# Kernel optimization log

Hardware: AMD Instinct MI355X
Metric: run time of the kernel (lower is better)

## Reference

```python
import jax, jax.numpy as jnp
import numpy as np
import math

B, T, D, H = 2, 2048, 1024, 16


def _layernorm(x, gamma, beta, eps=1e-5):
    mu = jnp.mean(x, axis=-1, keepdims=True)
    var = jnp.var(x, axis=-1, keepdims=True)
    return (x - mu) * jax.lax.rsqrt(var + eps) * gamma + beta


def setup_inputs() -> dict:
    key = jax.random.key(0)
    ks = jax.random.split(key, 12)
    s = 1.0 / math.sqrt(D)
    return {
        "x": jax.random.normal(ks[0], (B, T, D), dtype=jnp.float32),
        "src_mask": jax.random.randint(ks[1], (B, T, T), 0, 2, dtype=jnp.int32),
        "ln_gamma": jnp.ones((D,), jnp.float32),
        "ln_beta": jnp.zeros((D,), jnp.float32),
        "Wq": jax.random.normal(ks[2], (D, D), jnp.float32) * s,
        "bq": jnp.zeros((D,), jnp.float32),
        "Wk": jax.random.normal(ks[3], (D, D), jnp.float32) * s,
        "bk": jnp.zeros((D,), jnp.float32),
        "Wv": jax.random.normal(ks[4], (D, D), jnp.float32) * s,
        "bv": jnp.zeros((D,), jnp.float32),
        "Wo": jax.random.normal(ks[5], (D, D), jnp.float32) * s,
        "bo": jnp.zeros((D,), jnp.float32),
    }


def reference(x, src_mask, ln_gamma, ln_beta, Wq, bq, Wk, bk, Wv, bv, Wo, bo):
    Bx, Tx, Dx = x.shape
    dh = Dx // H
    xn = _layernorm(x, ln_gamma, ln_beta)  # single LN; the three calls are identical
    q = (xn @ Wq + bq).reshape(Bx, Tx, H, dh)
    k = (xn @ Wk + bk).reshape(Bx, Tx, H, dh)
    v = (xn @ Wv + bv).reshape(Bx, Tx, H, dh)
    # scores: B, n, m, h
    attn = jnp.einsum('bnhd,bmhd->bnmh', q, k) / math.sqrt(dh)
    attn = attn + (1.0 - src_mask.astype(attn.dtype))[..., None] * -100000.0
    weight = jax.nn.softmax(attn, axis=2)
    y = jnp.einsum('bnmh,bmhd->bnhd', weight, v).reshape(Bx, Tx, Dx)
    return x + (y @ Wo + bo)
```

## Files before the change

kernel.cpp:

```cpp
#include <hip/hip_runtime.h>
#include <hip/hip_bf16.h>
#include <stdint.h>

#define Tq 2048
#define Dd 1024
#define Hh 16

typedef unsigned short u16;
typedef __attribute__((ext_vector_type(8))) short short8;
typedef __attribute__((ext_vector_type(4))) float f32x4;

__device__ __forceinline__ u16 f2bf(float f) {
  union { float f; unsigned u; } v; v.f = f;
  unsigned r = (v.u + 0x7fffu + ((v.u >> 16) & 1u)) >> 16;
  return (u16)r;
}

__device__ __forceinline__ unsigned pk2bf(float a, float b) {
  __hip_bfloat162 h = __float22bfloat162_rn(float2{a, b});
  union { __hip_bfloat162 h; unsigned u; } c; c.h = h;
  return c.u;
}

__device__ __forceinline__ void load_lds16(const void* g, void* l) {
  __builtin_amdgcn_global_load_lds(
      (const __attribute__((address_space(1))) unsigned*)g,
      (__attribute__((address_space(3))) unsigned*)l, 16, 0, 0);
}

__device__ __forceinline__ f32x4 mfma16(short8 a, short8 b, f32x4 c) {
  return __builtin_amdgcn_mfma_f32_16x16x32_bf16(a, b, c, 0, 0, 0);
}

__global__ __launch_bounds__(256) void prep_kernel(
    const float* __restrict__ x, const float* __restrict__ gamma,
    const float* __restrict__ beta, u16* __restrict__ xn,
    const float* __restrict__ W0, const float* __restrict__ W1,
    const float* __restrict__ W2, const float* __restrict__ W3,
    u16* __restrict__ o_qkv, u16* __restrict__ o_o,
    const int* __restrict__ mask, uint32_t* __restrict__ bits,
    const float* __restrict__ bq, const float* __restrict__ bk,
    const float* __restrict__ bv, float* __restrict__ bias3) {
  __shared__ float t[32][33];
  int idx = blockIdx.x;
  int tid = threadIdx.x;
  if (idx < 4096) {
    int row = idx;
    const float4 v = ((const float4*)(x + (size_t)row * Dd))[tid];
    float s = v.x + v.y + v.z + v.w;
    float s2 = v.x * v.x + v.y * v.y + v.z * v.z + v.w * v.w;
#pragma unroll
    for (int off = 1; off < 64; off <<= 1) {
      s += __shfl_xor(s, off);
      s2 += __shfl_xor(s2, off);
    }
    int w = tid >> 6;
    if ((tid & 63) == 0) { t[0][w] = s; t[0][4 + w] = s2; }
    __syncthreads();
    s = t[0][0] + t[0][1] + t[0][2] + t[0][3];
    s2 = t[0][4] + t[0][5] + t[0][6] + t[0][7];
    float mu = s * (1.0f / Dd);
    float var = s2 * (1.0f / Dd) - mu * mu;
    float rstd = rsqrtf(var + 1e-5f);
    const float4 g = ((const float4*)gamma)[tid];
    const float4 bb = ((const float4*)beta)[tid];
    union { unsigned us[2]; uint2 u2; } o;
    o.us[0] = pk2bf((v.x - mu) * rstd * g.x + bb.x, (v.y - mu) * rstd * g.y + bb.y);
    o.us[1] = pk2bf((v.z - mu) * rstd * g.z + bb.z, (v.w - mu) * rstd * g.w + bb.w);
    *(uint2*)(xn + (size_t)row * Dd + tid * 4) = o.u2;
  } else if (idx < 8192) {
    int ti = idx - 4096;
    int z = ti >> 10, i = ti & 1023;
    const float* W = (z == 0) ? W0 : (z == 1) ? W1 : (z == 2) ? W2 : W3;
    u16* out = (z < 3) ? (o_qkv + (size_t)z * 1024 * 1024) : o_o;
    int k0 = (i & 31) * 32, n0 = (i >> 5) * 32;
    int tx = tid & 31, ty = tid >> 5;
#pragma unroll
    for (int j = 0; j < 4; ++j)
      t[ty + j * 8][tx] = W[(size_t)(k0 + ty + j * 8) * Dd + n0 + tx];
    __syncthreads();
#pragma unroll
    for (int j = 0; j < 4; ++j)
      out[(size_t)(n0 + ty + j * 8) * Dd + k0 + tx] = f2bf(t[tx][ty + j * 8]);
  } else if (idx < 9216) {
    int m = idx - 8192;
    int b = m >> 9, rest = m & 511;
    int qw = rest >> 3, kblk = rest & 7;
    int k = kblk * 256 + tid;
    const int* mp = mask + ((size_t)b * Tq + qw * 32) * Tq + k;
    uint32_t wv = 0;
#pragma unroll
    for (int j = 0; j < 32; ++j) wv |= (mp[(size_t)j * Tq] ? 1u : 0u) << j;
    bits[((size_t)b * 64 + qw) * Tq + k] = wv;
  } else {
    int i = (idx - 9216) * 256 + tid;
    float v = (i < 1024) ? bq[i] : (i < 2048) ? bk[i - 1024] : bv[i - 2048];
    bias3[i] = v;
  }
}

__global__ __launch_bounds__(256) void vt_kernel(
    const u16* __restrict__ qkv, u16* __restrict__ vt) {
  __shared__ u16 t[32][33];
  int bh = blockIdx.z;
  int b = bh >> 4, h = bh & 15;
  int t0 = blockIdx.x * 32, d0 = blockIdx.y * 32;
  int tx = threadIdx.x & 31, ty = threadIdx.x >> 5;
#pragma unroll
  for (int i = 0; i < 4; ++i)
    t[ty + i * 8][tx] =
        qkv[(size_t)(b * Tq + t0 + ty + i * 8) * 3072 + 2048 + h * 64 + d0 + tx];
  __syncthreads();
#pragma unroll
  for (int i = 0; i < 4; ++i)
    vt[((size_t)bh * 64 + d0 + ty + i * 8) * Tq + t0 + tx] = t[tx][ty + i * 8];
}

template <int MODE, int MT>
__global__ __launch_bounds__(256) void gemm_bt(
    const u16* __restrict__ A, const u16* __restrict__ Bt,
    const float* __restrict__ bias, const float* __restrict__ resid,
    void* __restrict__ Cout, int ldc, int K) {
  constexpr int MTI = MT / 32;
  constexpr int ACALLS = MT / 64;
  __shared__ u16 As[MT * 32];
  __shared__ u16 Bs[128 * 32];
  int tid = threadIdx.x;
  int lane = tid & 63, w = tid >> 6;
  int l16 = lane & 15, quad = lane >> 4;
  int wm = w >> 1, wn = w & 1;
  int m0 = blockIdx.y * MT, n0 = blockIdx.x * 128;
  int srow = lane >> 2, scol = (lane & 3) << 3;
  const u16* ga0 = A + (size_t)(m0 + srow) * K + scol;
  const u16* gb0 = Bt + (size_t)(n0 + srow) * K + scol;
  f32x4 acc[MTI][4];
#pragma unroll
  for (int i = 0; i < MTI; ++i)
#pragma unroll
    for (int j = 0; j < 4; ++j) acc[i][j] = {0.f, 0.f, 0.f, 0.f};

  for (int k0 = 0; k0 < K; k0 += 32) {
    __syncthreads();
#pragma unroll
    for (int c = 0; c < ACALLS; ++c) {
      int rb = w * (MT / 4) + c * 16;
      load_lds16(ga0 + (size_t)rb * K + k0, (char*)As + rb * 64);
    }
#pragma unroll
    for (int c = 0; c < 2; ++c) {
      int rb = w * 32 + c * 16;
      load_lds16(gb0 + (size_t)rb * K + k0, (char*)Bs + rb * 64);
    }
    __syncthreads();
    short8 af[MTI], bf[4];
#pragma unroll
    for (int mt = 0; mt < MTI; ++mt)
      af[mt] = *(const short8*)&As[(wm * (MT / 2) + mt * 16 + l16) * 32 + quad * 8];
#pragma unroll
    for (int nt = 0; nt < 4; ++nt)
      bf[nt] = *(const short8*)&Bs[(wn * 64 + nt * 16 + l16) * 32 + quad * 8];
#pragma unroll
    for (int mt = 0; mt < MTI; ++mt)
#pragma unroll
      for (int nt = 0; nt < 4; ++nt)
        acc[mt][nt] = mfma16(af[mt], bf[nt], acc[mt][nt]);
  }
#pragma unroll
  for (int nt = 0; nt < 4; ++nt) {
    int col = n0 + wn * 64 + nt * 16 + l16;
    float bv = bias[col];
    float scl = (MODE == 0 && col < 1024) ? 0.125f : 1.0f;
#pragma unroll
    for (int mt = 0; mt < MTI; ++mt) {
#pragma unroll
      for (int r = 0; r < 4; ++r) {
        int row = m0 + wm * (MT / 2) + mt * 16 + quad * 4 + r;
        size_t idx = (size_t)row * ldc + col;
        float vv = (acc[mt][nt][r] + bv) * scl;
        if (MODE == 0)
          ((u16*)Cout)[idx] = f2bf(vv);
        else
          ((float*)Cout)[idx] = vv + resid[idx];
      }
    }
  }
}

__global__ __launch_bounds__(256, 2) void attn_kernel(
    const u16* __restrict__ qkv, const u16* __restrict__ vt,
    const uint32_t* __restrict__ mbits, u16* __restrict__ ybuf) {
  __shared__ u16 Ks[2][64 * 64];
  __shared__ u16 Vs[2][64 * 64];
  __shared__ u16 Plds[4][32 * 64];
  int tid = threadIdx.x;
  int lane = tid & 63, w = tid >> 6;
  int l16 = lane & 15, quad = lane >> 4;
  int x7 = l16 & 7;
  int qt = blockIdx.x, h = blockIdx.y, b = blockIdx.z;
  int qbase = qt * 128 + w * 32;
  const u16* Qb = qkv + (size_t)b * Tq * 3072 + h * 64;
  const u16* Kb = Qb + 1024;
  const u16* Vb = vt + ((size_t)(b * Hh + h)) * 64 * Tq;
  const uint32_t* Mrow = mbits + ((size_t)b * 64 + (qbase >> 5)) * Tq;
  u16* Pw = Plds[w];

  int half = (w & 1) * 32;
  int r8 = lane >> 3;
  int phys = lane & 7;
  int chunk = phys ^ r8;
  bool isK = (w < 2);

  short8 qf[2][2];
#pragma unroll
  for (int nt = 0; nt < 2; ++nt)
#pragma unroll
    for (int ks = 0; ks < 2; ++ks)
      qf[nt][ks] = *(const short8*)&Qb[(size_t)(qbase + nt * 16 + l16) * 3072 +
                                       ks * 32 + quad * 8];

  f32x4 acc[2][4];
#pragma unroll
  for (int i = 0; i < 2; ++i)
#pragma unroll
    for (int j = 0; j < 4; ++j) acc[i][j] = {0.f, 0.f, 0.f, 0.f};
  float lst[2] = {0.f, 0.f};

  auto stage = [&](int buf, int k0) {
    if (isK) {
#pragma unroll
      for (int j = 0; j < 4; ++j)
        load_lds16(Kb + (size_t)(k0 + half + j * 8 + r8) * 3072 + chunk * 8,
                   (char*)&Ks[buf][0] + (half + j * 8) * 128);
    } else {
#pragma unroll
      for (int j = 0; j < 4; ++j)
        load_lds16(Vb + (size_t)(half + j * 8 + r8) * Tq + k0 + chunk * 8,
                   (char*)&Vs[buf][0] + (half + j * 8) * 128);
    }
  };

  stage(0, 0);

  for (int kt = 0; kt < 32; ++kt) {
    int k0 = kt * 64;
    int buf = kt & 1;
    __syncthreads();
    uint32_t mv[4][4];
#pragma unroll
    for (int mt = 0; mt < 4; ++mt) {
      uint4 m4 = *(const uint4*)&Mrow[k0 + mt * 16 + quad * 4];
      mv[mt][0] = m4.x; mv[mt][1] = m4.y; mv[mt][2] = m4.z; mv[mt][3] = m4.w;
    }
    if (kt < 31) stage(buf ^ 1, k0 + 64);
    const u16* Kt = Ks[buf];
    const u16* Vtile = Vs[buf];
    f32x4 s[4][2];
#pragma unroll
    for (int i = 0; i < 4; ++i)
#pragma unroll
      for (int j = 0; j < 2; ++j) s[i][j] = {0.f, 0.f, 0.f, 0.f};
#pragma unroll
    for (int mt = 0; mt < 4; ++mt)
#pragma unroll
      for (int ks = 0; ks < 2; ++ks) {
        short8 kf = *(const short8*)&Kt[(mt * 16 + l16) * 64 +
                                        (((ks << 2) | quad) ^ x7) * 8];
#pragma unroll
        for (int nt = 0; nt < 2; ++nt)
          s[mt][nt] = mfma16(kf, qf[nt][ks], s[mt][nt]);
      }
#pragma unroll
    for (int nt = 0; nt < 2; ++nt) {
      int shift = nt * 16 + l16;
#pragma unroll
      for (int mt = 0; mt < 4; ++mt) {
#pragma unroll
        for (int r = 0; r < 4; ++r) {
          float sv = ((mv[mt][r] >> shift) & 1u) ? s[mt][nt][r] : -100000.0f;
          float p = __expf(sv);
          s[mt][nt][r] = p;
          lst[nt] += p;
        }
        union { unsigned us[2]; uint2 u2; } pk;
        pk.us[0] = pk2bf(s[mt][nt][0], s[mt][nt][1]);
        pk.us[1] = pk2bf(s[mt][nt][2], s[mt][nt][3]);
        int p16 = (mt * 2 + (quad >> 1)) ^ x7;
        *(uint2*)&Pw[(nt * 16 + l16) * 64 + p16 * 8 + (quad & 1) * 4] = pk.u2;
      }
    }
    short8 pf[2][2];
#pragma unroll
    for (int mt2 = 0; mt2 < 2; ++mt2)
#pragma unroll
      for (int ks = 0; ks < 2; ++ks)
        pf[mt2][ks] = *(const short8*)&Pw[(mt2 * 16 + l16) * 64 +
                                          (((ks << 2) | quad) ^ x7) * 8];
#pragma unroll
    for (int ks = 0; ks < 2; ++ks)
#pragma unroll
      for (int nt2 = 0; nt2 < 4; ++nt2) {
        short8 vf = *(const short8*)&Vtile[(nt2 * 16 + l16) * 64 +
                                           (((ks << 2) | quad) ^ x7) * 8];
#pragma unroll
        for (int mt2 = 0; mt2 < 2; ++mt2)
          acc[mt2][nt2] = mfma16(pf[mt2][ks], vf, acc[mt2][nt2]);
      }
  }
#pragma unroll
  for (int nt = 0; nt < 2; ++nt) {
    lst[nt] += __shfl_xor(lst[nt], 16);
    lst[nt] += __shfl_xor(lst[nt], 32);
  }
#pragma unroll
  for (int mt2 = 0; mt2 < 2; ++mt2)
#pragma unroll
    for (int r = 0; r < 4; ++r) {
      float li = 1.0f / __shfl(lst[mt2], quad * 4 + r);
      size_t row = (size_t)b * Tq + qbase + mt2 * 16 + quad * 4 + r;
#pragma unroll
      for (int nt2 = 0; nt2 < 4; ++nt2)
        ybuf[row * Dd + h * 64 + nt2 * 16 + l16] = f2bf(acc[mt2][nt2][r] * li);
    }
}

extern "C" void kernel_launch(void* const* d_in, const int* in_sizes, int n_in,
                              void* d_out, int out_size, void* d_ws, size_t ws_size,
                              hipStream_t stream) {
  (void)in_sizes; (void)n_in; (void)out_size; (void)ws_size;
  const float* x = (const float*)d_in[0];
  const int* mask = (const int*)d_in[1];
  const float* gamma = (const float*)d_in[2];
  const float* beta = (const float*)d_in[3];
  const float* Wq = (const float*)d_in[4];
  const float* bq = (const float*)d_in[5];
  const float* Wk = (const float*)d_in[6];
  const float* bk = (const float*)d_in[7];
  const float* Wv = (const float*)d_in[8];
  const float* bv = (const float*)d_in[9];
  const float* Wo = (const float*)d_in[10];
  const float* bo = (const float*)d_in[11];
  float* out = (float*)d_out;
  char* ws = (char*)d_ws;

  constexpr size_t SZ_XN = (size_t)4096 * 1024 * 2;
  constexpr size_t SZ_WTQ = (size_t)3072 * 1024 * 2;
  constexpr size_t SZ_WOT = (size_t)1024 * 1024 * 2;
  constexpr size_t SZ_B3 = 3072 * 4;
  constexpr size_t SZ_QKV = (size_t)4096 * 3072 * 2;
  constexpr size_t SZ_MBITS = (size_t)2 * 64 * 2048 * 4;
  constexpr size_t SZ_VT = (size_t)2 * 16 * 64 * 2048 * 2;
  size_t off = 0;
  u16* xn = (u16*)(ws + off); off += SZ_XN;
  u16* wtqkv = (u16*)(ws + off); off += SZ_WTQ;
  u16* wot = (u16*)(ws + off); off += SZ_WOT;
  float* bias3 = (float*)(ws + off); off += SZ_B3;
  u16* qkvb = (u16*)(ws + off); off += SZ_QKV;
  uint32_t* mbits = (uint32_t*)(ws + off); off += SZ_MBITS;
  u16* vtb = (u16*)(ws + off); off += SZ_VT;
  u16* ybuf = (u16*)(ws + off);

  prep_kernel<<<dim3(9228), dim3(256), 0, stream>>>(
      x, gamma, beta, xn, Wq, Wk, Wv, Wo, wtqkv, wot, mask, mbits, bq, bk, bv,
      bias3);
  gemm_bt<0, 128><<<dim3(24, 32), dim3(256), 0, stream>>>(
      xn, wtqkv, bias3, nullptr, qkvb, 3072, 1024);
  vt_kernel<<<dim3(64, 2, 32), dim3(256), 0, stream>>>(qkvb, vtb);
  attn_kernel<<<dim3(16, 16, 2), dim3(256), 0, stream>>>(qkvb, vtb, mbits, ybuf);
  gemm_bt<1, 64><<<dim3(8, 64), dim3(256), 0, stream>>>(
      ybuf, wot, bo, x, out, 1024, 1024);
}
```

Baseline: 246.0 us.

## Split attention over key halves, add combine kernel, widen GEMM K-tile

Measured after the change: 255.9 us. +4.0%, slower.

```diff
diff --git a/kernel.cpp b/kernel.cpp
--- a/kernel.cpp
+++ b/kernel.cpp
@@ -122,54 +122,66 @@
     const float* __restrict__ bias, const float* __restrict__ resid,
     void* __restrict__ Cout, int ldc, int K) {
   constexpr int MTI = MT / 32;
-  constexpr int ACALLS = MT / 64;
-  __shared__ u16 As[MT * 32];
-  __shared__ u16 Bs[128 * 32];
+  __shared__ u16 As[MT * 64];
+  __shared__ u16 Bs[128 * 64];
   int tid = threadIdx.x;
   int lane = tid & 63, w = tid >> 6;
   int l16 = lane & 15, quad = lane >> 4;
+  int x7 = l16 & 7;
   int wm = w >> 1, wn = w & 1;
   int m0 = blockIdx.y * MT, n0 = blockIdx.x * 128;
-  int srow = lane >> 2, scol = (lane & 3) << 3;
-  const u16* ga0 = A + (size_t)(m0 + srow) * K + scol;
-  const u16* gb0 = Bt + (size_t)(n0 + srow) * K + scol;
+  int r8 = lane >> 3;
+  int phys = lane & 7;
+  int chunk = phys ^ r8;
+  const u16* ga0 = A + (size_t)(m0 + r8) * K + chunk * 8;
+  const u16* gb0 = Bt + (size_t)(n0 + r8) * K + chunk * 8;
   f32x4 acc[MTI][4];
 #pragma unroll
   for (int i = 0; i < MTI; ++i)
 #pragma unroll
     for (int j = 0; j < 4; ++j) acc[i][j] = {0.f, 0.f, 0.f, 0.f};
 
-  for (int k0 = 0; k0 < K; k0 += 32) {
+  for (int k0 = 0; k0 < K; k0 += 64) {
     __syncthreads();
 #pragma unroll
-    for (int c = 0; c < ACALLS; ++c) {
-      int rb = w * (MT / 4) + c * 16;
-      load_lds16(ga0 + (size_t)rb * K + k0, (char*)As + rb * 64);
-    }
-#pragma unroll
-    for (int c = 0; c < 2; ++c) {
-      int rb = w * 32 + c * 16;
-      load_lds16(gb0 + (size_t)rb * K + k0, (char*)Bs + rb * 64);
+    for (int c = 0; c < MT / 32; ++c) {
+      int rb = c * 32 + w * 8;
+      load_lds16(ga0 + (size_t)rb * K + k0, (char*)As + rb * 128);
+    }
+#pragma unroll
+    for (int c = 0; c < 4; ++c) {
+      int rb = c * 32 + w * 8;
+      load_lds16(gb0 + (size_t)rb * K + k0, (char*)Bs + rb * 128);
     }
     __syncthreads();
-    short8 af[MTI], bf[4];
-#pragma unroll
-    for (int mt = 0; mt < MTI; ++mt)
-      af[mt] = *(const short8*)&As[(wm * (MT / 2) + mt * 16 + l16) * 32 + quad * 8];
-#pragma unroll
-    for (int nt = 0; nt < 4; ++nt)
-      bf[nt] = *(const short8*)&Bs[(wn * 64 + nt * 16 + l16) * 32 + quad * 8];
-#pragma unroll
-    for (int mt = 0; mt < MTI; ++mt)
-#pragma unroll
-      for (int nt = 0; nt < 4; ++nt)
-        acc[mt][nt] = mfma16(af[mt], bf[nt], acc[mt][nt]);
+    short8 af[MTI][2], bf[4][2];
+#pragma unroll
+    for (int mt = 0; mt < MTI; ++mt) {
+      int row = wm * (MT / 2) + mt * 16 + l16;
+#pragma unroll
+      for (int ks = 0; ks < 2; ++ks)
+        af[mt][ks] = *(const short8*)&As[row * 64 + (((ks << 2) | quad) ^ x7) * 8];
+    }
+#pragma unroll
+    for (int nt = 0; nt < 4; ++nt) {
+      int row = wn * 64 + nt * 16 + l16;
+#pragma unroll
+      for (int ks = 0; ks < 2; ++ks)
+        bf[nt][ks] = *(const short8*)&Bs[row * 64 + (((ks << 2) | quad) ^ x7) * 8];
+    }
+#pragma unroll
+    for (int ks = 0; ks < 2; ++ks)
+#pragma unroll
+      for (int mt = 0; mt < MTI; ++mt)
+#pragma unroll
+        for (int nt = 0; nt < 4; ++nt)
+          acc[mt][nt] = mfma16(af[mt][ks], bf[nt][ks], acc[mt][nt]);
   }
 #pragma unroll
   for (int nt = 0; nt < 4; ++nt) {
     int col = n0 + wn * 64 + nt * 16 + l16;
     float bv = bias[col];
-    float scl = (MODE == 0 && col < 1024) ? 0.125f : 1.0f;
+    float scl = (MODE == 0 && col < 1024) ? 0.18033688011112042f : 1.0f;
 #pragma unroll
     for (int mt = 0; mt < MTI; ++mt) {
 #pragma unroll
@@ -186,9 +198,10 @@
   }
 }
 
-__global__ __launch_bounds__(256, 2) void attn_kernel(
+__global__ __launch_bounds__(256, 3) void attn_kernel(
     const u16* __restrict__ qkv, const u16* __restrict__ vt,
-    const uint32_t* __restrict__ mbits, u16* __restrict__ ybuf) {
+    const uint32_t* __restrict__ mbits, float* __restrict__ ubuf,
+    float* __restrict__ lbuf) {
   __shared__ u16 Ks[2][64 * 64];
   __shared__ u16 Vs[2][64 * 64];
   __shared__ u16 Plds[4][32 * 64];
@@ -196,8 +209,12 @@
   int lane = tid & 63, w = tid >> 6;
   int l16 = lane & 15, quad = lane >> 4;
   int x7 = l16 & 7;
-  int qt = blockIdx.x, h = blockIdx.y, b = blockIdx.z;
+  int qt = blockIdx.x;
+  int hs = blockIdx.y;
+  int h = hs >> 1, split = hs & 1;
+  int b = blockIdx.z;
   int qbase = qt * 128 + w * 32;
+  int kbase = split << 10;
   const u16* Qb = qkv + (size_t)b * Tq * 3072 + h * 64;
   const u16* Kb = Qb + 1024;
   const u16* Vb = vt + ((size_t)(b * Hh + h)) * 64 * Tq;
@@ -239,10 +256,10 @@
     }
   };
 
-  stage(0, 0);
-
-  for (int kt = 0; kt < 32; ++kt) {
-    int k0 = kt * 64;
+  stage(0, kbase);
+
+  for (int kt = 0; kt < 16; ++kt) {
+    int k0 = kbase + kt * 64;
     int buf = kt & 1;
     __syncthreads();
     uint32_t mv[4][4];
@@ -251,7 +268,7 @@
       uint4 m4 = *(const uint4*)&Mrow[k0 + mt * 16 + quad * 4];
       mv[mt][0] = m4.x; mv[mt][1] = m4.y; mv[mt][2] = m4.z; mv[mt][3] = m4.w;
     }
-    if (kt < 31) stage(buf ^ 1, k0 + 64);
+    if (kt < 15) stage(buf ^ 1, k0 + 64);
     const u16* Kt = Ks[buf];
     const u16* Vtile = Vs[buf];
     f32x4 s[4][2];
@@ -277,7 +294,7 @@
 #pragma unroll
         for (int r = 0; r < 4; ++r) {
           float sv = ((mv[mt][r] >> shift) & 1u) ? s[mt][nt][r] : -100000.0f;
-          float p = __expf(sv);
+          float p = exp2f(sv);
           s[mt][nt][r] = p;
           lst[nt] += p;
         }
@@ -315,12 +332,35 @@
   for (int mt2 = 0; mt2 < 2; ++mt2)
 #pragma unroll
     for (int r = 0; r < 4; ++r) {
-      float li = 1.0f / __shfl(lst[mt2], quad * 4 + r);
-      size_t row = (size_t)b * Tq + qbase + mt2 * 16 + quad * 4 + r;
+      int q = qbase + mt2 * 16 + quad * 4 + r;
+      size_t ro = ((size_t)split * 4096 + b * Tq + q) * Dd + h * 64;
 #pragma unroll
       for (int nt2 = 0; nt2 < 4; ++nt2)
-        ybuf[row * Dd + h * 64 + nt2 * 16 + l16] = f2bf(acc[mt2][nt2][r] * li);
-    }
+        ubuf[ro + nt2 * 16 + l16] = acc[mt2][nt2][r];
+    }
+  if (quad == 0) {
+#pragma unroll
+    for (int nt = 0; nt < 2; ++nt) {
+      int q = qbase + nt * 16 + l16;
+      lbuf[((size_t)split * 4096 + b * Tq + q) * Hh + h] = lst[nt];
+    }
+  }
+}
+
+__global__ __launch_bounds__(256) void combine_kernel(
+    const float* __restrict__ u, const float* __restrict__ lb,
+    u16* __restrict__ ybuf) {
+  int row = blockIdx.x;
+  int c = threadIdx.x * 4;
+  float4 a = *(const float4*)&u[(size_t)row * Dd + c];
+  float4 d = *(const float4*)&u[(size_t)(4096 + row) * Dd + c];
+  int h = c >> 6;
+  float l = lb[(size_t)row * Hh + h] + lb[(size_t)(4096 + row) * Hh + h];
+  float inv = 1.0f / l;
+  union { unsigned us[2]; uint2 u2; } o;
+  o.us[0] = pk2bf((a.x + d.x) * inv, (a.y + d.y) * inv);
+  o.us[1] = pk2bf((a.z + d.z) * inv, (a.w + d.w) * inv);
+  *(uint2*)&ybuf[(size_t)row * Dd + c] = o.u2;
 }
 
 extern "C" void kernel_launch(void* const* d_in, const int* in_sizes, int n_in,
@@ -342,22 +382,24 @@
   float* out = (float*)d_out;
   char* ws = (char*)d_ws;
 
-  constexpr size_t SZ_XN = (size_t)4096 * 1024 * 2;
-  constexpr size_t SZ_WTQ = (size_t)3072 * 1024 * 2;
+  constexpr size_t SZ_U = (size_t)2 * 4096 * 1024 * 4;
   constexpr size_t SZ_WOT = (size_t)1024 * 1024 * 2;
   constexpr size_t SZ_B3 = 3072 * 4;
-  constexpr size_t SZ_QKV = (size_t)4096 * 3072 * 2;
   constexpr size_t SZ_MBITS = (size_t)2 * 64 * 2048 * 4;
   constexpr size_t SZ_VT = (size_t)2 * 16 * 64 * 2048 * 2;
+  constexpr size_t SZ_L = (size_t)2 * 4096 * 16 * 4;
   size_t off = 0;
-  u16* xn = (u16*)(ws + off); off += SZ_XN;
-  u16* wtqkv = (u16*)(ws + off); off += SZ_WTQ;
+  float* ubuf = (float*)(ws + off);
+  u16* xn = (u16*)(ws + off);
+  u16* wtqkv = (u16*)(ws + off + (size_t)4096 * 1024 * 2);
+  off += SZ_U;
   u16* wot = (u16*)(ws + off); off += SZ_WOT;
   float* bias3 = (float*)(ws + off); off += SZ_B3;
-  u16* qkvb = (u16*)(ws + off); off += SZ_QKV;
   uint32_t* mbits = (uint32_t*)(ws + off); off += SZ_MBITS;
   u16* vtb = (u16*)(ws + off); off += SZ_VT;
-  u16* ybuf = (u16*)(ws + off);
+  float* lbuf = (float*)(ws + off); off += SZ_L;
+  u16* qkvb = (u16*)(ws + off);
+  u16* ybuf = qkvb;
 
   prep_kernel<<<dim3(9228), dim3(256), 0, stream>>>(
       x, gamma, beta, xn, Wq, Wk, Wv, Wo, wtqkv, wot, mask, mbits, bq, bk, bv,
@@ -365,7 +407,9 @@
   gemm_bt<0, 128><<<dim3(24, 32), dim3(256), 0, stream>>>(
       xn, wtqkv, bias3, nullptr, qkvb, 3072, 1024);
   vt_kernel<<<dim3(64, 2, 32), dim3(256), 0, stream>>>(qkvb, vtb);
-  attn_kernel<<<dim3(16, 16, 2), dim3(256), 0, stream>>>(qkvb, vtb, mbits, ybuf);
+  attn_kernel<<<dim3(16, 32, 2), dim3(256), 0, stream>>>(qkvb, vtb, mbits, ubuf,
+                                                         lbuf);
+  combine_kernel<<<dim3(4096), dim3(256), 0, stream>>>(ubuf, lbuf, ybuf);
   gemm_bt<1, 64><<<dim3(8, 64), dim3(256), 0, stream>>>(
       ybuf, wot, bo, x, out, 1024, 1024);
 }
```
